# Kernel optimization log

Measured on AMD Instinct MI355X. Metric: run time of the kernel, lower is better.

## Reference

```python
import jax, jax.numpy as jnp
import numpy as np

# bitsandbytes NF4 codebook (16 levels, normalized to [-1, 1])
NF4_CODE = jnp.array([
    -1.0, -0.6961928009986877, -0.5250730514526367, -0.39491748809814453,
    -0.28444138169288635, -0.18477343022823334, -0.09105003625154495, 0.0,
    0.07958029955625534, 0.16093020141124725, 0.24611230194568634,
    0.33791524171829224, 0.44070982933044434, 0.5626170039176941,
    0.7229568362236023, 1.0], dtype=jnp.float32)

BLOCK = 64  # bitsandbytes default quantization blocksize
TOK, DIN, DOUT, RANK = 8192, 4096, 4096, 16
LORA_ALPHA = 16
SCALING = LORA_ALPHA / RANK ** 0.5  # rslora


def setup_inputs() -> dict:
    key = jax.random.key(0)
    k1, k2, k3, k4, k5, k6 = jax.random.split(key, 6)
    x = jax.random.normal(k1, (TOK, DIN), dtype=jnp.float32)
    w_codes = jax.random.randint(k2, (DOUT, DIN), 0, 16, dtype=jnp.int32)
    absmax = jax.random.uniform(k3, (DOUT, DIN // BLOCK), dtype=jnp.float32)
    bias = jax.random.normal(k4, (DOUT,), dtype=jnp.float32)
    lora_A = jax.random.normal(k5, (DIN, RANK), dtype=jnp.float32) * (1.0 / DIN ** 0.5)
    lora_B = jax.random.normal(k6, (RANK, DOUT), dtype=jnp.float32) * 0.02
    return {"x": x, "w_codes": w_codes, "absmax": absmax, "bias": bias,
            "lora_A": lora_A, "lora_B": lora_B}


def reference(x, w_codes, absmax, bias, lora_A, lora_B):
    # Dequantize NF4 base weight: codebook lookup * per-block absmax scale
    # W: [DOUT, DIN], absmax broadcast over blocks of 64 along DIN
    W = NF4_CODE[w_codes] * jnp.repeat(absmax, BLOCK, axis=1)
    base_out = x @ W.T + bias                      # [TOK, DOUT]
    lora_out = (x @ lora_A) @ lora_B               # low-rank path [TOK, DOUT]
    return base_out + lora_out * SCALING
```

## Files before the change

kernel.cpp:

```cpp
#include <hip/hip_runtime.h>
#include <hip/hip_bf16.h>
#include <cstdint>
#include <cstddef>

#define TOK   8192
#define DIN   4096
#define DOUT  4096
#define RANK  16
#define KE    4160
#define NKT64 (KE / 64)

#define BM 256
#define BN 256

typedef __attribute__((ext_vector_type(8))) short bf16x8;
typedef __attribute__((ext_vector_type(4))) float f32x4;
typedef __attribute__((ext_vector_type(8))) unsigned short u16x8;

__device__ __constant__ float NF4_CODE_D[16] = {
    -1.0f, -0.6961928009986877f, -0.5250730514526367f, -0.39491748809814453f,
    -0.28444138169288635f, -0.18477343022823334f, -0.09105003625154495f, 0.0f,
    0.07958029955625534f, 0.16093020141124725f, 0.24611230194568634f,
    0.33791524171829224f, 0.44070982933044434f, 0.5626170039176941f,
    0.7229568362236023f, 1.0f};

__device__ __forceinline__ unsigned short f2bf(float f) {
    union { float f; unsigned u; } v; v.f = f;
    unsigned u = v.u;
    unsigned r = (u + 0x7FFFu + ((u >> 16) & 1u)) >> 16;
    return (unsigned short)r;
}

__device__ __forceinline__ void async_copy16(const void* g, void* l) {
    __builtin_amdgcn_global_load_lds(
        (const __attribute__((address_space(1))) void*)g,
        (__attribute__((address_space(3))) void*)l,
        16, 0, 0);
}

__global__ __launch_bounds__(256) void prep_x(const float* __restrict__ x,
                                              const float* __restrict__ lora_A,
                                              unsigned short* __restrict__ xe) {
    const int tid = threadIdx.x;
    const int l = tid & 63;
    const int w = tid >> 6;
    const int t0 = blockIdx.x * 16 + w * 4;

    float p[4][16];
#pragma unroll
    for (int a = 0; a < 4; ++a)
#pragma unroll
        for (int r = 0; r < 16; ++r) p[a][r] = 0.f;

    for (int it = 0; it < 16; ++it) {
        const int kb = it * 256 + l * 4;
        float4 xv[4];
#pragma unroll
        for (int a = 0; a < 4; ++a)
            xv[a] = *(const float4*)(x + (size_t)(t0 + a) * DIN + kb);
#pragma unroll
        for (int a = 0; a < 4; ++a) {
            ushort4 s;
            s.x = f2bf(xv[a].x); s.y = f2bf(xv[a].y);
            s.z = f2bf(xv[a].z); s.w = f2bf(xv[a].w);
            *(ushort4*)(xe + (size_t)(t0 + a) * KE + kb) = s;
        }
#pragma unroll
        for (int j = 0; j < 4; ++j) {
            const float4* ap = (const float4*)(lora_A + (size_t)(kb + j) * RANK);
            const float4 a0 = ap[0], a1 = ap[1], a2 = ap[2], a3 = ap[3];
            const float av[16] = {a0.x, a0.y, a0.z, a0.w, a1.x, a1.y, a1.z, a1.w,
                                  a2.x, a2.y, a2.z, a2.w, a3.x, a3.y, a3.z, a3.w};
#pragma unroll
            for (int a = 0; a < 4; ++a) {
                const float xs = (j == 0) ? xv[a].x : (j == 1) ? xv[a].y
                                : (j == 2) ? xv[a].z : xv[a].w;
#pragma unroll
                for (int r = 0; r < 16; ++r) p[a][r] += xs * av[r];
            }
        }
    }

#pragma unroll
    for (int a = 0; a < 4; ++a) {
#pragma unroll
        for (int r = 0; r < 16; ++r) {
            float v = p[a][r];
#pragma unroll
            for (int off = 32; off > 0; off >>= 1) v += __shfl_xor(v, off, 64);
            if (l == r)
                xe[(size_t)(t0 + a) * KE + DIN + r] = f2bf(4.0f * v);
        }
        if (l >= 16)
            xe[(size_t)(t0 + a) * KE + DIN + l] =
                (l == 16) ? (unsigned short)0x3F80u : (unsigned short)0u;
    }
}

__global__ __launch_bounds__(256) void dequant_w(const int* __restrict__ codes,
                                                 const float* __restrict__ absmax,
                                                 unsigned short* __restrict__ we) {
    __shared__ float tab[16];
    if (threadIdx.x < 16) tab[threadIdx.x] = NF4_CODE_D[threadIdx.x];
    __syncthreads();
    const size_t tid = (size_t)blockIdx.x * 256 + threadIdx.x;
    const size_t base = tid * 8;
    const int o = (int)(base >> 12);
    const int k = (int)(base & (DIN - 1));
    const float am = absmax[base >> 6];
    const int4 c0 = *(const int4*)(codes + base);
    const int4 c1 = *(const int4*)(codes + base + 4);
    u16x8 ov;
    ov[0] = f2bf(tab[c0.x] * am);
    ov[1] = f2bf(tab[c0.y] * am);
    ov[2] = f2bf(tab[c0.z] * am);
    ov[3] = f2bf(tab[c0.w] * am);
    ov[4] = f2bf(tab[c1.x] * am);
    ov[5] = f2bf(tab[c1.y] * am);
    ov[6] = f2bf(tab[c1.z] * am);
    ov[7] = f2bf(tab[c1.w] * am);
    *(u16x8*)(we + (size_t)o * KE + k) = ov;
}

__global__ __launch_bounds__(256) void fill_wtail(const float* __restrict__ lora_B,
                                                  const float* __restrict__ bias,
                                                  unsigned short* __restrict__ we) {
    const int o = blockIdx.x * 256 + threadIdx.x;
    if (o >= DOUT) return;
    unsigned short* dst = we + (size_t)o * KE + DIN;
#pragma unroll
    for (int r = 0; r < RANK; ++r) dst[r] = f2bf(lora_B[(size_t)r * DOUT + o]);
    dst[16] = f2bf(bias[o]);
#pragma unroll
    for (int r = 17; r < 64; ++r) dst[r] = 0;
}

__global__ __launch_bounds__(512, 2) void gemm_bt(const unsigned short* __restrict__ A,
                                                  const unsigned short* __restrict__ B,
                                                  float* __restrict__ C) {
    __shared__ __attribute__((aligned(1024))) char smem[4 * 32768];

    const int tid = threadIdx.x;
    const int l = tid & 63;
    const int w = tid >> 6;
    const int wm = w >> 2;
    const int wn = w & 3;

    const int tm = blockIdx.x >> 4;
    const int tn = blockIdx.x & 15;
    const int rowBase = tm * BM;
    const int colBase = tn * BN;

    int srow[2], scolb[2], loffs[2];
#pragma unroll
    for (int g = 0; g < 2; ++g) {
        const int loff = g * 8192 + tid * 16;
        const int soff = loff ^ (((loff >> 7) & 7) << 4);
        loffs[g] = loff;
        srow[g] = soff >> 6;
        scolb[g] = soff & 63;
    }

    auto stageA = [&](int tt, int kh, int slot) {
        char* dst = smem + slot * 32768;
        const int k0 = tt * 64 + kh * 32;
#pragma unroll
        for (int g = 0; g < 2; ++g)
            async_copy16((const char*)A + ((size_t)(rowBase + srow[g]) * KE + k0) * 2 + scolb[g],
                         dst + loffs[g]);
    };
    auto stageB = [&](int tt, int kh, int slot) {
        char* dst = smem + slot * 32768 + 16384;
        const int k0 = tt * 64 + kh * 32;
#pragma unroll
        for (int g = 0; g < 2; ++g)
            async_copy16((const char*)B + ((size_t)(colBase + srow[g]) * KE + k0) * 2 + scolb[g],
                         dst + loffs[g]);
    };

    const int lmask = ((l >> 1) & 7) << 4;
    const int aoff = (((wm * 128 + (l & 15)) * 64) + ((l >> 4) * 16)) ^ lmask;
    const int boff = (((wn * 64 + (l & 15)) * 64) + ((l >> 4) * 16)) ^ lmask;

    f32x4 acc[8][4];
#pragma unroll
    for (int m = 0; m < 8; ++m)
#pragma unroll
        for (int n = 0; n < 4; ++n) acc[m][n] = (f32x4){0.f, 0.f, 0.f, 0.f};

    bf16x8 aLo[4], aHi[4], aLo2[4], aHi2[4], bCur[4], bNxt[4];

    stageA(0, 0, 0); stageB(0, 0, 0);
    stageA(0, 1, 1); stageB(0, 1, 1);
    asm volatile("s_waitcnt vmcnt(4)" ::: "memory");
    __builtin_amdgcn_s_barrier();
    {
        const char* S0 = smem;
#pragma unroll
        for (int n = 0; n < 4; ++n)
            bCur[n] = *(const bf16x8*)(S0 + 16384 + boff + n * 1024);
#pragma unroll
        for (int m = 0; m < 4; ++m)
            aLo[m] = *(const bf16x8*)(S0 + aoff + m * 1024);
    }

    for (int t = 0; t < NKT64; ++t) {
        const char* S0 = smem + ((2 * t) & 3) * 32768;
        const char* S1 = smem + ((2 * t + 1) & 3) * 32768;
        const char* Sn = smem + ((2 * t + 2) & 3) * 32768;
        const int d0 = (2 * t + 2) & 3, d1 = (2 * t + 3) & 3;
        const bool more = (t + 1 < NKT64);

#pragma unroll
        for (int m = 0; m < 4; ++m)
            aHi[m] = *(const bf16x8*)(S0 + aoff + (4 + m) * 1024);
        if (more) stageA(t + 1, 0, d0);
        __builtin_amdgcn_sched_barrier(0);
        __builtin_amdgcn_s_setprio(1);
#pragma unroll
        for (int m = 0; m < 4; ++m)
#pragma unroll
            for (int n = 0; n < 4; ++n)
                acc[m][n] = __builtin_amdgcn_mfma_f32_16x16x32_bf16(
                    aLo[m], bCur[n], acc[m][n], 0, 0, 0);
        __builtin_amdgcn_s_setprio(0);
        __builtin_amdgcn_sched_barrier(0);

        if (more) {
            asm volatile("s_waitcnt vmcnt(2)" ::: "memory");
        } else {
            asm volatile("s_waitcnt vmcnt(0)" ::: "memory");
        }
        __builtin_amdgcn_s_barrier();
        __builtin_amdgcn_sched_barrier(0);
#pragma unroll
        for (int n = 0; n < 4; ++n)
            bNxt[n] = *(const bf16x8*)(S1 + 16384 + boff + n * 1024);
#pragma unroll
        for (int m = 0; m < 4; ++m)
            aLo2[m] = *(const bf16x8*)(S1 + aoff + m * 1024);
        if (more) stageB(t + 1, 0, d0);
        __builtin_amdgcn_sched_barrier(0);
        __builtin_amdgcn_s_setprio(1);
#pragma unroll
        for (int m = 0; m < 4; ++m)
#pragma unroll
            for (int n = 0; n < 4; ++n)
                acc[4 + m][n] = __builtin_amdgcn_mfma_f32_16x16x32_bf16(
                    aHi[m], bCur[n], acc[4 + m][n], 0, 0, 0);
        __builtin_amdgcn_s_setprio(0);
        __builtin_amdgcn_sched_barrier(0);

#pragma unroll
        for (int m = 0; m < 4; ++m)
            aHi2[m] = *(const bf16x8*)(S1 + aoff + (4 + m) * 1024);
        if (more) stageA(t + 1, 1, d1);
        __builtin_amdgcn_sched_barrier(0);
        __builtin_amdgcn_s_setprio(1);
#pragma unroll
        for (int m = 0; m < 4; ++m)
#pragma unroll
            for (int n = 0; n < 4; ++n)
                acc[m][n] = __builtin_amdgcn_mfma_f32_16x16x32_bf16(
                    aLo2[m], bNxt[n], acc[m][n], 0, 0, 0);
        __builtin_amdgcn_s_setprio(0);
        __builtin_amdgcn_sched_barrier(0);

        if (more) {
            asm volatile("s_waitcnt vmcnt(2)" ::: "memory");
            __builtin_amdgcn_s_barrier();
            __builtin_amdgcn_sched_barrier(0);
#pragma unroll
            for (int n = 0; n < 4; ++n)
                bCur[n] = *(const bf16x8*)(Sn + 16384 + boff + n * 1024);
#pragma unroll
            for (int m = 0; m < 4; ++m)
                aLo[m] = *(const bf16x8*)(Sn + aoff + m * 1024);
            stageB(t + 1, 1, d1);
        }
        __builtin_amdgcn_sched_barrier(0);
        __builtin_amdgcn_s_setprio(1);
#pragma unroll
        for (int m = 0; m < 4; ++m)
#pragma unroll
            for (int n = 0; n < 4; ++n)
                acc[4 + m][n] = __builtin_amdgcn_mfma_f32_16x16x32_bf16(
                    aHi2[m], bNxt[n], acc[4 + m][n], 0, 0, 0);
        __builtin_amdgcn_s_setprio(0);
        __builtin_amdgcn_sched_barrier(0);
    }

#pragma unroll
    for (int m = 0; m < 8; ++m) {
        const int rowg = rowBase + wm * 128 + m * 16 + (l >> 4) * 4;
#pragma unroll
        for (int n = 0; n < 4; ++n) {
            const int colg = colBase + wn * 64 + n * 16 + (l & 15);
            float* cp = C + (size_t)rowg * DOUT + colg;
#pragma unroll
            for (int r = 0; r < 4; ++r) cp[(size_t)r * DOUT] = acc[m][n][r];
        }
    }
}

extern "C" void kernel_launch(void* const* d_in, const int* in_sizes, int n_in,
                              void* d_out, int out_size, void* d_ws, size_t ws_size,
                              hipStream_t stream) {
    const float* x      = (const float*)d_in[0];
    const int*   codes  = (const int*)d_in[1];
    const float* absmax = (const float*)d_in[2];
    const float* bias   = (const float*)d_in[3];
    const float* lora_A = (const float*)d_in[4];
    const float* lora_B = (const float*)d_in[5];
    float* out = (float*)d_out;

    unsigned short* xe = (unsigned short*)d_ws;
    unsigned short* we = xe + (size_t)TOK * KE;

    prep_x<<<TOK / 16, 256, 0, stream>>>(x, lora_A, xe);
    dequant_w<<<(DOUT * (size_t)DIN / 8) / 256, 256, 0, stream>>>(codes, absmax, we);
    fill_wtail<<<DOUT / 256, 256, 0, stream>>>(lora_B, bias, we);
    gemm_bt<<<(TOK / BM) * (DOUT / BN), 512, 0, stream>>>(xe, we, out);
}
```

Before: 362.4 us.

## Fuse prep kernels into one launch and issue A/B stages together in GEMM

Merges the three preprocessing kernels (x conversion with LoRA-A projection, NF4 dequant, weight tail fill) into a single launch that dispatches on block index, removing two launch gaps and letting the independent work overlap. In the GEMM main loop, the B-tile async loads are now issued alongside the A-tile loads, and the vmcnt wait threshold is raised to match, so global loads go out earlier. In exchange, more loads are in flight at each point in the loop, and the __syncthreads in the dequant branch only runs in that branch, which is uniform per block so it is safe.

```diff
diff --git a/kernel.cpp b/kernel.cpp
--- a/kernel.cpp
+++ b/kernel.cpp
@@ -13,6 +13,10 @@
 #define BM 256
 #define BN 256
 
+#define PXB 512
+#define DQB 8192
+#define TLB 16
+
 typedef __attribute__((ext_vector_type(8))) short bf16x8;
 typedef __attribute__((ext_vector_type(4))) float f32x4;
 typedef __attribute__((ext_vector_type(8))) unsigned short u16x8;
@@ -38,101 +42,98 @@
         16, 0, 0);
 }
 
-__global__ __launch_bounds__(256) void prep_x(const float* __restrict__ x,
-                                              const float* __restrict__ lora_A,
-                                              unsigned short* __restrict__ xe) {
+__global__ __launch_bounds__(256) void prep_fused(
+        const float* __restrict__ x, const float* __restrict__ lora_A,
+        const int* __restrict__ codes, const float* __restrict__ absmax,
+        const float* __restrict__ bias, const float* __restrict__ lora_B,
+        unsigned short* __restrict__ xe, unsigned short* __restrict__ we) {
+    __shared__ float tab[16];
+    const int bid = blockIdx.x;
     const int tid = threadIdx.x;
-    const int l = tid & 63;
-    const int w = tid >> 6;
-    const int t0 = blockIdx.x * 16 + w * 4;
-
-    float p[4][16];
-#pragma unroll
-    for (int a = 0; a < 4; ++a)
-#pragma unroll
-        for (int r = 0; r < 16; ++r) p[a][r] = 0.f;
-
-    for (int it = 0; it < 16; ++it) {
-        const int kb = it * 256 + l * 4;
-        float4 xv[4];
+
+    if (bid < PXB) {
+        const int l = tid & 63;
+        const int w = tid >> 6;
+        const int t0 = bid * 16 + w * 4;
+
+        float p[4][16];
 #pragma unroll
         for (int a = 0; a < 4; ++a)
-            xv[a] = *(const float4*)(x + (size_t)(t0 + a) * DIN + kb);
+#pragma unroll
+            for (int r = 0; r < 16; ++r) p[a][r] = 0.f;
+
+        for (int it = 0; it < 16; ++it) {
+            const int kb = it * 256 + l * 4;
+            float4 xv[4];
+#pragma unroll
+            for (int a = 0; a < 4; ++a)
+                xv[a] = *(const float4*)(x + (size_t)(t0 + a) * DIN + kb);
+#pragma unroll
+            for (int a = 0; a < 4; ++a) {
+                ushort4 s;
+                s.x = f2bf(xv[a].x); s.y = f2bf(xv[a].y);
+                s.z = f2bf(xv[a].z); s.w = f2bf(xv[a].w);
+                *(ushort4*)(xe + (size_t)(t0 + a) * KE + kb) = s;
+            }
+#pragma unroll
+            for (int j = 0; j < 4; ++j) {
+                const float4* ap = (const float4*)(lora_A + (size_t)(kb + j) * RANK);
+                const float4 a0 = ap[0], a1 = ap[1], a2 = ap[2], a3 = ap[3];
+                const float av[16] = {a0.x, a0.y, a0.z, a0.w, a1.x, a1.y, a1.z, a1.w,
+                                      a2.x, a2.y, a2.z, a2.w, a3.x, a3.y, a3.z, a3.w};
+#pragma unroll
+                for (int a = 0; a < 4; ++a) {
+                    const float xs = (j == 0) ? xv[a].x : (j == 1) ? xv[a].y
+                                    : (j == 2) ? xv[a].z : xv[a].w;
+#pragma unroll
+                    for (int r = 0; r < 16; ++r) p[a][r] += xs * av[r];
+                }
+            }
+        }
+
 #pragma unroll
         for (int a = 0; a < 4; ++a) {
-            ushort4 s;
-            s.x = f2bf(xv[a].x); s.y = f2bf(xv[a].y);
-            s.z = f2bf(xv[a].z); s.w = f2bf(xv[a].w);
-            *(ushort4*)(xe + (size_t)(t0 + a) * KE + kb) = s;
-        }
-#pragma unroll
-        for (int j = 0; j < 4; ++j) {
-            const float4* ap = (const float4*)(lora_A + (size_t)(kb + j) * RANK);
-            const float4 a0 = ap[0], a1 = ap[1], a2 = ap[2], a3 = ap[3];
-            const float av[16] = {a0.x, a0.y, a0.z, a0.w, a1.x, a1.y, a1.z, a1.w,
-                                  a2.x, a2.y, a2.z, a2.w, a3.x, a3.y, a3.z, a3.w};
-#pragma unroll
-            for (int a = 0; a < 4; ++a) {
-                const float xs = (j == 0) ? xv[a].x : (j == 1) ? xv[a].y
-                                : (j == 2) ? xv[a].z : xv[a].w;
-#pragma unroll
-                for (int r = 0; r < 16; ++r) p[a][r] += xs * av[r];
+#pragma unroll
+            for (int r = 0; r < 16; ++r) {
+                float v = p[a][r];
+#pragma unroll
+                for (int off = 32; off > 0; off >>= 1) v += __shfl_xor(v, off, 64);
+                if (l == r)
+                    xe[(size_t)(t0 + a) * KE + DIN + r] = f2bf(4.0f * v);
             }
-        }
-    }
-
-#pragma unroll
-    for (int a = 0; a < 4; ++a) {
-#pragma unroll
-        for (int r = 0; r < 16; ++r) {
-            float v = p[a][r];
-#pragma unroll
-            for (int off = 32; off > 0; off >>= 1) v += __shfl_xor(v, off, 64);
-            if (l == r)
-                xe[(size_t)(t0 + a) * KE + DIN + r] = f2bf(4.0f * v);
-        }
-        if (l >= 16)
-            xe[(size_t)(t0 + a) * KE + DIN + l] =
-                (l == 16) ? (unsigned short)0x3F80u : (unsigned short)0u;
-    }
-}
-
-__global__ __launch_bounds__(256) void dequant_w(const int* __restrict__ codes,
-                                                 const float* __restrict__ absmax,
-                                                 unsigned short* __restrict__ we) {
-    __shared__ float tab[16];
-    if (threadIdx.x < 16) tab[threadIdx.x] = NF4_CODE_D[threadIdx.x];
-    __syncthreads();
-    const size_t tid = (size_t)blockIdx.x * 256 + threadIdx.x;
-    const size_t base = tid * 8;
-    const int o = (int)(base >> 12);
-    const int k = (int)(base & (DIN - 1));
-    const float am = absmax[base >> 6];
-    const int4 c0 = *(const int4*)(codes + base);
-    const int4 c1 = *(const int4*)(codes + base + 4);
-    u16x8 ov;
-    ov[0] = f2bf(tab[c0.x] * am);
-    ov[1] = f2bf(tab[c0.y] * am);
-    ov[2] = f2bf(tab[c0.z] * am);
-    ov[3] = f2bf(tab[c0.w] * am);
-    ov[4] = f2bf(tab[c1.x] * am);
-    ov[5] = f2bf(tab[c1.y] * am);
-    ov[6] = f2bf(tab[c1.z] * am);
-    ov[7] = f2bf(tab[c1.w] * am);
-    *(u16x8*)(we + (size_t)o * KE + k) = ov;
-}
-
-__global__ __launch_bounds__(256) void fill_wtail(const float* __restrict__ lora_B,
-                                                  const float* __restrict__ bias,
-                                                  unsigned short* __restrict__ we) {
-    const int o = blockIdx.x * 256 + threadIdx.x;
-    if (o >= DOUT) return;
-    unsigned short* dst = we + (size_t)o * KE + DIN;
-#pragma unroll
-    for (int r = 0; r < RANK; ++r) dst[r] = f2bf(lora_B[(size_t)r * DOUT + o]);
-    dst[16] = f2bf(bias[o]);
-#pragma unroll
-    for (int r = 17; r < 64; ++r) dst[r] = 0;
+            if (l >= 16)
+                xe[(size_t)(t0 + a) * KE + DIN + l] =
+                    (l == 16) ? (unsigned short)0x3F80u : (unsigned short)0u;
+        }
+    } else if (bid < PXB + DQB) {
+        if (tid < 16) tab[tid] = NF4_CODE_D[tid];
+        __syncthreads();
+        const size_t t = (size_t)(bid - PXB) * 256 + tid;
+        const size_t base = t * 8;
+        const int o = (int)(base >> 12);
+        const int k = (int)(base & (DIN - 1));
+        const float am = absmax[base >> 6];
+        const int4 c0 = *(const int4*)(codes + base);
+        const int4 c1 = *(const int4*)(codes + base + 4);
+        u16x8 ov;
+        ov[0] = f2bf(tab[c0.x] * am);
+        ov[1] = f2bf(tab[c0.y] * am);
+        ov[2] = f2bf(tab[c0.z] * am);
+        ov[3] = f2bf(tab[c0.w] * am);
+        ov[4] = f2bf(tab[c1.x] * am);
+        ov[5] = f2bf(tab[c1.y] * am);
+        ov[6] = f2bf(tab[c1.z] * am);
+        ov[7] = f2bf(tab[c1.w] * am);
+        *(u16x8*)(we + (size_t)o * KE + k) = ov;
+    } else {
+        const int o = (bid - PXB - DQB) * 256 + tid;
+        unsigned short* dst = we + (size_t)o * KE + DIN;
+#pragma unroll
+        for (int r = 0; r < RANK; ++r) dst[r] = f2bf(lora_B[(size_t)r * DOUT + o]);
+        dst[16] = f2bf(bias[o]);
+#pragma unroll
+        for (int r = 17; r < 64; ++r) dst[r] = 0;
+    }
 }
 
 __global__ __launch_bounds__(512, 2) void gemm_bt(const unsigned short* __restrict__ A,
@@ -214,7 +215,7 @@
 #pragma unroll
         for (int m = 0; m < 4; ++m)
             aHi[m] = *(const bf16x8*)(S0 + aoff + (4 + m) * 1024);
-        if (more) stageA(t + 1, 0, d0);
+        if (more) { stageA(t + 1, 0, d0); stageB(t + 1, 0, d0); }
         __builtin_amdgcn_sched_barrier(0);
         __builtin_amdgcn_s_setprio(1);
 #pragma unroll
@@ -227,7 +228,7 @@
         __builtin_amdgcn_sched_barrier(0);
 
         if (more) {
-            asm volatile("s_waitcnt vmcnt(2)" ::: "memory");
+            asm volatile("s_waitcnt vmcnt(4)" ::: "memory");
         } else {
             asm volatile("s_waitcnt vmcnt(0)" ::: "memory");
         }
@@ -239,7 +240,6 @@
 #pragma unroll
         for (int m = 0; m < 4; ++m)
             aLo2[m] = *(const bf16x8*)(S1 + aoff + m * 1024);
-        if (more) stageB(t + 1, 0, d0);
         __builtin_amdgcn_sched_barrier(0);
         __builtin_amdgcn_s_setprio(1);
 #pragma unroll
@@ -254,7 +254,7 @@
 #pragma unroll
         for (int m = 0; m < 4; ++m)
             aHi2[m] = *(const bf16x8*)(S1 + aoff + (4 + m) * 1024);
-        if (more) stageA(t + 1, 1, d1);
+        if (more) { stageA(t + 1, 1, d1); stageB(t + 1, 1, d1); }
         __builtin_amdgcn_sched_barrier(0);
         __builtin_amdgcn_s_setprio(1);
 #pragma unroll
@@ -267,7 +267,7 @@
         __builtin_amdgcn_sched_barrier(0);
 
         if (more) {
-            asm volatile("s_waitcnt vmcnt(2)" ::: "memory");
+            asm volatile("s_waitcnt vmcnt(4)" ::: "memory");
             __builtin_amdgcn_s_barrier();
             __builtin_amdgcn_sched_barrier(0);
 #pragma unroll
@@ -276,7 +276,6 @@
 #pragma unroll
             for (int m = 0; m < 4; ++m)
                 aLo[m] = *(const bf16x8*)(Sn + aoff + m * 1024);
-            stageB(t + 1, 1, d1);
         }
         __builtin_amdgcn_sched_barrier(0);
         __builtin_amdgcn_s_setprio(1);
@@ -317,8 +316,7 @@
     unsigned short* xe = (unsigned short*)d_ws;
     unsigned short* we = xe + (size_t)TOK * KE;
 
-    prep_x<<<TOK / 16, 256, 0, stream>>>(x, lora_A, xe);
-    dequant_w<<<(DOUT * (size_t)DIN / 8) / 256, 256, 0, stream>>>(codes, absmax, we);
-    fill_wtail<<<DOUT / 256, 256, 0, stream>>>(lora_B, bias, we);
+    prep_fused<<<PXB + DQB + TLB, 256, 0, stream>>>(x, lora_A, codes, absmax,
+                                                    bias, lora_B, xe, we);
     gemm_bt<<<(TOK / BM) * (DOUT / BN), 512, 0, stream>>>(xe, we, out);
 }
```

Measured after the change: 356.0 us. No clear change (-1.8%).
